# Kernel optimization log

Hardware: AMD Instinct MI355X
Metric: run time of the kernel (lower is better)

Reference implementation:

```python
import jax, jax.numpy as jnp
import numpy as np

B, T, N, H, DH = 32, 64, 100, 4, 32  # batch, seq, nodes, heads, dim/head


def setup_inputs() -> dict:
    key = jax.random.key(0)
    ks = jax.random.split(key, 20)
    # structured flat observation: [action_mask(132), adj(100*100), dt(1), obs(256), siem(128)]
    am = (jax.random.uniform(ks[0], (B, T, 132)) < 0.8).astype(jnp.float32)
    adj = (jax.random.uniform(ks[1], (B, T, N * N)) < 0.05).astype(jnp.float32)
    dt = jax.random.uniform(ks[2], (B, T, 1)) * 0.1 + 0.01
    obs = jax.random.normal(ks[3], (B, T, 256))
    siem = jax.random.normal(ks[4], (B, T, 128))
    inputs = jnp.concatenate([am, adj, dt, obs, siem], axis=-1)
    s = 0.05
    return dict(
        inputs=inputs,
        h0=jnp.zeros((B, 128), jnp.float32),
        fc_w=jax.random.normal(ks[5], (384, 256)) * s,
        fc_b=jnp.zeros((256,)),
        gat_w=jax.random.normal(ks[6], (256, H, DH)) * s,
        a_src=jax.random.normal(ks[7], (H, DH)) * s,
        a_dst=jax.random.normal(ks[8], (H, DH)) * s,
        ode_w1=jax.random.normal(ks[9], (128, 128)) * s,
        ode_b1=jnp.zeros((128,)),
        ode_w2=jax.random.normal(ks[10], (128, 128)) * s,
        ode_b2=jnp.zeros((128,)),
        gru_wi=jax.random.normal(ks[11], (128, 384)) * s,
        gru_wh=jax.random.normal(ks[12], (128, 384)) * s,
        gru_bi=jnp.zeros((384,)),
        gru_bh=jnp.zeros((384,)),
        act_w=jax.random.normal(ks[13], (128, 132)) * s,
        act_b=jnp.zeros((132,)),
        val_w=jax.random.normal(ks[14], (128, 1)) * s,
        val_b=jnp.zeros((1,)),
    )


def reference(inputs, h0, fc_w, fc_b, gat_w, a_src, a_dst, ode_w1, ode_b1,
              ode_w2, ode_b2, gru_wi, gru_wh, gru_bi, gru_bh, act_w, act_b,
              val_w, val_b):
    Bt, Tt = inputs.shape[0], inputs.shape[1]
    action_mask = inputs[..., :132]
    adj_raw = inputs[..., 132:10132].reshape(Bt * Tt, N, N)
    dtn = inputs[..., 10132:10133]                      # [B,T,1]
    x = jnp.concatenate([inputs[..., 10133:10389], inputs[..., 10389:10517]], -1)
    x = jax.nn.relu(x @ fc_w + fc_b).reshape(Bt * Tt, 256)
    # SubnetMaskGenerator.create_mask: binary adjacency + self loops
    adj = (adj_raw > 0) | jnp.eye(N, dtype=bool)[None]
    # place per-agent embedding at node 0, rest zero
    x_nodes = jnp.zeros((Bt * Tt, N, 256), x.dtype).at[:, 0, :].set(x)
    Wh = jnp.einsum('bnf,fhd->bhnd', x_nodes, gat_w)
    src = jnp.einsum('bhnd,hd->bhn', Wh, a_src)
    dst = jnp.einsum('bhnd,hd->bhn', Wh, a_dst)
    e = jax.nn.leaky_relu(src[:, :, :, None] + dst[:, :, None, :], 0.2)
    e = jnp.where(adj[:, None, :, :], e, -1e9)
    alpha = jax.nn.softmax(e, axis=-1)
    hgat = jax.nn.elu(jnp.einsum('bhij,bhjd->bhid', alpha, Wh))
    hgat = hgat.transpose(0, 2, 1, 3).reshape(Bt * Tt, N, H * DH)
    x_gat = hgat.mean(axis=1).reshape(Bt, Tt, 128)

    def f(h):  # ODE dynamics net
        return jnp.tanh(jnp.tanh(h @ ode_w1 + ode_b1) @ ode_w2 + ode_b2)

    def step(h, inp):
        xt, dt = inp                                    # [B,128], [B,1]
        k1 = f(h)
        k2 = f(h + 0.5 * dt * k1)
        k3 = f(h + 0.5 * dt * k2)
        k4 = f(h + dt * k3)
        h_ode = h + dt / 6.0 * (k1 + 2 * k2 + 2 * k3 + k4)
        gi = xt @ gru_wi + gru_bi
        gh = h_ode @ gru_wh + gru_bh
        ir, iz, inn = jnp.split(gi, 3, -1)
        hr, hz, hn = jnp.split(gh, 3, -1)
        r = jax.nn.sigmoid(ir + hr)
        z = jax.nn.sigmoid(iz + hz)
        n = jnp.tanh(inn + r * hn)
        h_new = (1.0 - z) * n + z * h_ode
        return h_new, h_new

    h_T, hs = jax.lax.scan(step, h0, (x_gat.transpose(1, 0, 2), dtn.transpose(1, 0, 2)))
    x_rnn = hs.transpose(1, 0, 2)                       # [B,T,128]
    logits = x_rnn @ act_w + act_b
    value = (x_rnn @ val_w + val_b).reshape(-1)
    masked_logits = jnp.where(action_mask == 0.0, jnp.float32(-1e10), logits)
    return masked_logits, h_T, value
```

## Files before the change

### kernel.cpp

```cpp
#include <hip/hip_runtime.h>

#define NIN 10517
typedef unsigned short ushort_t;
using f32x4  = __attribute__((ext_vector_type(4))) float;
using bf16x8 = __attribute__((ext_vector_type(8))) short;

__device__ __forceinline__ float lrelu02(float x){ return x > 0.f ? x : 0.2f*x; }
__device__ __forceinline__ float fast_tanh(float x){ float e=__expf(2.f*x); return 1.f - 2.f/(e+1.f); }
__device__ __forceinline__ float fast_sig(float x){ return 1.f/(1.f+__expf(-x)); }

__device__ __forceinline__ ushort_t f2bf(float x){
  unsigned u = __float_as_uint(x);
  unsigned r = u + 0x7FFF + ((u >> 16) & 1);
  return (ushort_t)(r >> 16);
}
__device__ __forceinline__ float bf2f(ushort_t v){ return __uint_as_float(((unsigned)v) << 16); }

#define LBAR() do { asm volatile("s_waitcnt lgkmcnt(0)" ::: "memory"); \
                    __builtin_amdgcn_s_barrier(); } while (0)

__global__ __launch_bounds__(256) void k_fc_gat(const float* __restrict__ inputs,
    const float* __restrict__ fc_w, const float* __restrict__ fc_b,
    const float* __restrict__ gat_w, const float* __restrict__ a_src, const float* __restrict__ a_dst,
    const float* __restrict__ ode_w1, const float* __restrict__ ode_w2, const float* __restrict__ gru_wh,
    const float* __restrict__ act_w, const float* __restrict__ gru_wi,
    float* __restrict__ wh0_ws, float* __restrict__ sd_ws,
    ushort_t* __restrict__ w1B, ushort_t* __restrict__ w2B, ushort_t* __restrict__ ghB,
    ushort_t* __restrict__ actB, ushort_t* __restrict__ wiBt,
    ushort_t* __restrict__ fc_wB, ushort_t* __restrict__ gat_wB)
{
  __shared__ __align__(16) ushort_t xinB[16][392];
  __shared__ __align__(16) ushort_t xfcB[16][264];
  __shared__ float wh[16][132];
  const int tid = threadIdx.x;
  const int bt0 = blockIdx.x * 16;

  for (int p = blockIdx.x * 256 + tid; p < 280576; p += 128*256) {
    if (p < 49152) {
      int m = p >> 7, k = p & 127;
      ghB[p] = f2bf(gru_wh[k*384 + m]);
    } else if (p < 65536) {
      int q = p - 49152, jj = q >> 7, k = q & 127;
      w1B[q] = f2bf(ode_w1[k*128 + jj]);
    } else if (p < 81920) {
      int q = p - 65536, jj = q >> 7, k = q & 127;
      w2B[q] = f2bf(ode_w2[k*128 + jj]);
    } else if (p < 100352) {
      int q = p - 81920, col = q >> 7, k = q & 127;
      actB[q] = (col < 132) ? f2bf(act_w[k*132 + col]) : (ushort_t)0;
    } else if (p < 149504) {
      int q = p - 100352, m = q >> 7, f = q & 127;
      wiBt[q] = f2bf(gru_wi[f*384 + m]);
    } else if (p < 247808) {
      int q = p - 149504, col = q / 384, k = q - col*384;
      fc_wB[q] = f2bf(fc_w[k*256 + col]);
    } else {
      int q = p - 247808, col = q >> 8, k = q & 255;
      gat_wB[q] = f2bf(gat_w[k*128 + col]);
    }
  }

  for (int idx = tid; idx < 16*384; idx += 256) {
    int r = idx / 384, f = idx - r*384;
    xinB[r][f] = f2bf(inputs[(size_t)(bt0+r)*NIN + 10133 + f]);
  }
  __syncthreads();

  const int w = tid >> 6, lane = tid & 63;
  const int li = lane & 15, g = lane >> 4;

  {
    bf16x8 afr[12];
    #pragma unroll
    for (int kt=0;kt<12;kt++)
      afr[kt] = *reinterpret_cast<const bf16x8*>(&xinB[li][kt*32 + g*8]);
    for (int ct = w*4; ct < w*4 + 4; ct++) {
      f32x4 acc = {0.f,0.f,0.f,0.f};
      #pragma unroll
      for (int kt=0;kt<12;kt++){
        bf16x8 bf = *reinterpret_cast<const bf16x8*>(fc_wB + (size_t)(ct*16+li)*384 + kt*32 + g*8);
        acc = __builtin_amdgcn_mfma_f32_16x16x32_bf16(afr[kt], bf, acc, 0,0,0);
      }
      const float bias = fc_b[ct*16 + li];
      #pragma unroll
      for (int r=0;r<4;r++)
        xfcB[g*4 + r][ct*16 + li] = f2bf(fmaxf(acc[r] + bias, 0.f));
    }
  }
  __syncthreads();

  {
    bf16x8 afr[8];
    #pragma unroll
    for (int kt=0;kt<8;kt++)
      afr[kt] = *reinterpret_cast<const bf16x8*>(&xfcB[li][kt*32 + g*8]);
    for (int ct = w*2; ct < w*2 + 2; ct++) {
      f32x4 acc = {0.f,0.f,0.f,0.f};
      #pragma unroll
      for (int kt=0;kt<8;kt++){
        bf16x8 bf = *reinterpret_cast<const bf16x8*>(gat_wB + (size_t)(ct*16+li)*256 + kt*32 + g*8);
        acc = __builtin_amdgcn_mfma_f32_16x16x32_bf16(afr[kt], bf, acc, 0,0,0);
      }
      #pragma unroll
      for (int r=0;r<4;r++){
        const int row = g*4 + r, col = ct*16 + li;
        wh[row][col] = acc[r];
        wh0_ws[(size_t)(bt0+row)*128 + col] = acc[r];
      }
    }
  }
  __syncthreads();

  if (tid < 128) {
    const int r = tid >> 3, h = (tid >> 1) & 3, wv = tid & 1;
    const float* av = wv ? a_dst : a_src;
    float acc = 0.f;
    #pragma unroll
    for (int d=0; d<32; d++) acc = fmaf(wh[r][h*32+d], av[h*32+d], acc);
    sd_ws[(size_t)(bt0+r)*8 + wv*4 + h] = acc;
  }
}

__global__ __launch_bounds__(256) void k_alpha_gi(const float* __restrict__ inputs,
    const float* __restrict__ wh0_ws, const float* __restrict__ sd_ws,
    ushort_t* __restrict__ xg_bf)
{
  __shared__ int cnt[100];
  __shared__ int a0f[100];
  __shared__ float alpha[4][100];
  __shared__ float wh0[128];
  __shared__ float sdl[8];
  __shared__ float psum[256];
  const int tid = threadIdx.x;
  const size_t bt = blockIdx.x;
  if (tid < 128) wh0[tid] = wh0_ws[bt*128 + tid];
  if (tid < 8) sdl[tid] = sd_ws[bt*8 + tid];
  const float* adj = inputs + bt*NIN + 132;
  const int wv = tid >> 6, lane = tid & 63;
  for (int i = wv; i < 100; i += 4) {
    float v0 = adj[i*100 + lane];
    int pred0 = (lane != 0) && ((v0 > 0.f) || (lane == i));
    unsigned long long b0 = __ballot(pred0);
    int pred1 = 0;
    if (lane < 36) {
      float v1 = adj[i*100 + 64 + lane];
      pred1 = (v1 > 0.f) || ((64 + lane) == i);
    }
    unsigned long long b1 = __ballot(pred1);
    if (lane == 0) {
      cnt[i] = __popcll(b0) + __popcll(b1);
      a0f[i] = (v0 > 0.f) ? 1 : 0;
    }
  }
  __syncthreads();
  for (int idx = tid; idx < 400; idx += 256) {
    int h = idx / 100, i = idx - h*100;
    float s = sdl[h], d = sdl[4+h];
    float a;
    if (i == 0) {
      float ea = __expf(lrelu02(s + d));
      float eb = __expf(lrelu02(s));
      a = ea / (ea + (float)cnt[0] * eb);
    } else if (a0f[i]) {
      float ed = __expf(lrelu02(d));
      a = ed / (ed + (float)cnt[i]);
    } else {
      a = 0.f;
    }
    alpha[h][i] = a;
  }
  __syncthreads();
  {
    const int pr = tid & 127, hf = tid >> 7;
    const float w = wh0[pr];
    const int hh = pr >> 5;
    float sum = 0.f;
    const int i0 = hf * 50;
    for (int i = i0; i < i0 + 50; i++) {
      float t = alpha[hh][i] * w;
      sum += (t > 0.f) ? t : (__expf(t) - 1.f);
    }
    psum[tid] = sum;
  }
  __syncthreads();
  if (tid < 128) xg_bf[bt*128 + tid] = f2bf((psum[tid] + psum[tid+128]) * 0.01f);
}

__global__ __launch_bounds__(256) void k_gi(const ushort_t* __restrict__ xg_bf,
    const ushort_t* __restrict__ wiBt, const float* __restrict__ gru_bi,
    float* __restrict__ gi_ws)
{
  const int tid = threadIdx.x;
  const int w = tid >> 6, lane = tid & 63;
  const int li = lane & 15, g = lane >> 4;
  const int bt0 = blockIdx.x * 16;
  bf16x8 haf[4];
  #pragma unroll
  for (int kt=0;kt<4;kt++)
    haf[kt] = *reinterpret_cast<const bf16x8*>(xg_bf + ((size_t)(bt0 + li))*128 + kt*32 + g*8);
  for (int ct = w*6; ct < w*6 + 6; ct++) {
    const int m = ct*16 + li;
    const f32x4 z0 = {0.f,0.f,0.f,0.f};
    const ushort_t* wb = wiBt + (size_t)m*128;
    bf16x8 b0 = *reinterpret_cast<const bf16x8*>(wb + 0*32 + g*8);
    bf16x8 b1f = *reinterpret_cast<const bf16x8*>(wb + 1*32 + g*8);
    bf16x8 b2f = *reinterpret_cast<const bf16x8*>(wb + 2*32 + g*8);
    bf16x8 b3f = *reinterpret_cast<const bf16x8*>(wb + 3*32 + g*8);
    f32x4 c0 = __builtin_amdgcn_mfma_f32_16x16x32_bf16(haf[0], b0,  z0, 0,0,0);
    f32x4 c1 = __builtin_amdgcn_mfma_f32_16x16x32_bf16(haf[1], b1f, z0, 0,0,0);
    f32x4 c2 = __builtin_amdgcn_mfma_f32_16x16x32_bf16(haf[2], b2f, z0, 0,0,0);
    f32x4 c3 = __builtin_amdgcn_mfma_f32_16x16x32_bf16(haf[3], b3f, z0, 0,0,0);
    const float bim = gru_bi[m];
    #pragma unroll
    for (int r=0;r<4;r++)
      gi_ws[(size_t)(bt0 + g*4 + r)*384 + m] = ((c0[r]+c1[r]) + (c2[r]+c3[r])) + bim;
  }
}

__global__ __launch_bounds__(512) void k_rnn(const float* __restrict__ inputs,
    const float* __restrict__ h0,
    const ushort_t* __restrict__ w1B, const float* __restrict__ ode_b1,
    const ushort_t* __restrict__ w2B, const float* __restrict__ ode_b2,
    const ushort_t* __restrict__ ghB, const float* __restrict__ gru_bh,
    const ushort_t* __restrict__ actB, const float* __restrict__ act_b,
    const float* __restrict__ val_w, const float* __restrict__ val_b,
    const float* __restrict__ gi_ws,
    float* __restrict__ out_logits, float* __restrict__ out_hT, float* __restrict__ out_val)
{
  __shared__ __align__(16) ushort_t bufA[128];
  __shared__ __align__(16) ushort_t bufB[128];
  __shared__ __align__(16) ushort_t bufC[128];
  __shared__ float dtbuf[64];
  __shared__ __align__(16) ushort_t hsbuf[64*136];
  const int tid = threadIdx.x;
  const int b = blockIdx.x;
  const int w = tid >> 6, lane = tid & 63;
  const int li = lane & 15, g = lane >> 4;
  const int col = w*16 + li;

  bf16x8 W1f[4], W2f[4], GAf[4], GBf[4], GCf[4];
  #pragma unroll
  for (int kt=0;kt<4;kt++){
    const int o = kt*32 + g*8;
    W1f[kt] = *reinterpret_cast<const bf16x8*>(w1B + col*128 + o);
    W2f[kt] = *reinterpret_cast<const bf16x8*>(w2B + col*128 + o);
    GAf[kt] = *reinterpret_cast<const bf16x8*>(ghB + (size_t)col*128       + o);
    GBf[kt] = *reinterpret_cast<const bf16x8*>(ghB + (size_t)(col+128)*128 + o);
    GCf[kt] = *reinterpret_cast<const bf16x8*>(ghB + (size_t)(col+256)*128 + o);
  }
  const float b1 = ode_b1[col], b2 = ode_b2[col];
  const float bh0 = gru_bh[col], bh1 = gru_bh[col+128], bh2 = gru_bh[col+256];
  float h = h0[b*128 + col];
  if (tid < 64) dtbuf[tid] = inputs[((size_t)b*64 + tid)*NIN + 10132];
  if (lane < 16) bufC[col] = f2bf(h);
  const float* gib = gi_ws + (size_t)b*64*384 + col;
  __syncthreads();

  bf16x8 af[4];
  auto ldaf = [&](const ushort_t* __restrict__ hb){
    #pragma unroll
    for (int kt=0;kt<4;kt++) af[kt] = *reinterpret_cast<const bf16x8*>(hb + kt*32 + g*8);
  };
  auto mvac = [&](const bf16x8 (&Wf)[4])->float{
    const f32x4 z0 = {0.f,0.f,0.f,0.f};
    f32x4 c0 = __builtin_amdgcn_mfma_f32_16x16x32_bf16(af[0], Wf[0], z0, 0,0,0);
    f32x4 c1 = __builtin_amdgcn_mfma_f32_16x16x32_bf16(af[1], Wf[1], z0, 0,0,0);
    f32x4 c2 = __builtin_amdgcn_mfma_f32_16x16x32_bf16(af[2], Wf[2], z0, 0,0,0);
    f32x4 c3 = __builtin_amdgcn_mfma_f32_16x16x32_bf16(af[3], Wf[3], z0, 0,0,0);
    return (c0[0]+c1[0]) + (c2[0]+c3[0]);
  };

  for (int t=0; t<64; t++) {
    const float dt = dtbuf[t];
    const float gir = gib[(size_t)t*384];
    const float giz = gib[(size_t)t*384 + 128];
    const float gin = gib[(size_t)t*384 + 256];

    float u, k1, k2, k3, k4;
    ldaf(bufC); u  = fast_tanh(mvac(W1f)+b1); if (lane<16) bufA[col]=f2bf(u);                    LBAR();
    ldaf(bufA); k1 = fast_tanh(mvac(W2f)+b2); if (lane<16) bufB[col]=f2bf(fmaf(0.5f*dt,k1,h));   LBAR();
    ldaf(bufB); u  = fast_tanh(mvac(W1f)+b1); if (lane<16) bufA[col]=f2bf(u);                    LBAR();
    ldaf(bufA); k2 = fast_tanh(mvac(W2f)+b2); if (lane<16) bufB[col]=f2bf(fmaf(0.5f*dt,k2,h));   LBAR();
    ldaf(bufB); u  = fast_tanh(mvac(W1f)+b1); if (lane<16) bufA[col]=f2bf(u);                    LBAR();
    ldaf(bufA); k3 = fast_tanh(mvac(W2f)+b2); if (lane<16) bufB[col]=f2bf(fmaf(dt,k3,h));        LBAR();
    ldaf(bufB); u  = fast_tanh(mvac(W1f)+b1); if (lane<16) bufA[col]=f2bf(u);                    LBAR();
    ldaf(bufA); k4 = fast_tanh(mvac(W2f)+b2);
    const float h_ode = fmaf(dt*(1.f/6.f), (k1 + 2.f*k2) + (2.f*k3 + k4), h);
    if (lane<16) bufB[col] = f2bf(h_ode);                                                        LBAR();

    ldaf(bufB);
    {
      const float r = fast_sig(gir + mvac(GAf) + bh0);
      const float z = fast_sig(giz + mvac(GBf) + bh1);
      const float n = fast_tanh(gin + r*(mvac(GCf) + bh2));
      h = (1.f - z)*n + z*h_ode;
    }
    if (lane < 16) {
      bufC[col] = f2bf(h);
      hsbuf[t*136 + col] = f2bf(h);
    }
    LBAR();
  }

  if (lane < 16) out_hT[b*128 + col] = h;

  {
    const int rt = w & 3, ch = w >> 2;
    const int r0 = rt*16;
    bf16x8 haf[4];
    #pragma unroll
    for (int kt=0;kt<4;kt++)
      haf[kt] = *reinterpret_cast<const bf16x8*>(hsbuf + (r0+li)*136 + kt*32 + g*8);
    const int ct0 = ch ? 5 : 0, ctN = ch ? 9 : 5;
    for (int ct=ct0; ct<ctN; ct++){
      const f32x4 z0 = {0.f,0.f,0.f,0.f};
      f32x4 c0, c1, c2, c3;
      {
        const ushort_t* ab = actB + (size_t)(ct*16+li)*128;
        bf16x8 b0 = *reinterpret_cast<const bf16x8*>(ab + 0*32 + g*8);
        bf16x8 b1f = *reinterpret_cast<const bf16x8*>(ab + 1*32 + g*8);
        bf16x8 b2f = *reinterpret_cast<const bf16x8*>(ab + 2*32 + g*8);
        bf16x8 b3f = *reinterpret_cast<const bf16x8*>(ab + 3*32 + g*8);
        c0 = __builtin_amdgcn_mfma_f32_16x16x32_bf16(haf[0], b0,  z0, 0,0,0);
        c1 = __builtin_amdgcn_mfma_f32_16x16x32_bf16(haf[1], b1f, z0, 0,0,0);
        c2 = __builtin_amdgcn_mfma_f32_16x16x32_bf16(haf[2], b2f, z0, 0,0,0);
        c3 = __builtin_amdgcn_mfma_f32_16x16x32_bf16(haf[3], b3f, z0, 0,0,0);
      }
      const int colL = ct*16 + li;
      if (colL < 132){
        const float ab = act_b[colL];
        #pragma unroll
        for (int reg=0; reg<4; reg++){
          const int r = r0 + g*4 + reg;
          const size_t bt = (size_t)b*64 + r;
          const float mval = inputs[bt*NIN + colL];
          const float v = ((c0[reg]+c1[reg]) + (c2[reg]+c3[reg])) + ab;
          out_logits[bt*132 + colL] = (mval == 0.f) ? -1e10f : v;
        }
      }
    }
  }
  if (tid < 64){
    float acc = val_b[0];
    for (int k=0;k<128;k++) acc = fmaf(bf2f(hsbuf[tid*136 + k]), val_w[k], acc);
    out_val[b*64 + tid] = acc;
  }
}

extern "C" void kernel_launch(void* const* d_in, const int* in_sizes, int n_in,
                              void* d_out, int out_size, void* d_ws, size_t ws_size,
                              hipStream_t stream) {
  (void)in_sizes; (void)n_in; (void)out_size; (void)ws_size;
  const float* inputs = (const float*)d_in[0];
  const float* h0     = (const float*)d_in[1];
  const float* fc_w   = (const float*)d_in[2];
  const float* fc_b   = (const float*)d_in[3];
  const float* gat_w  = (const float*)d_in[4];
  const float* a_src  = (const float*)d_in[5];
  const float* a_dst  = (const float*)d_in[6];
  const float* ode_w1 = (const float*)d_in[7];
  const float* ode_b1 = (const float*)d_in[8];
  const float* ode_w2 = (const float*)d_in[9];
  const float* ode_b2 = (const float*)d_in[10];
  const float* gru_wi = (const float*)d_in[11];
  const float* gru_wh = (const float*)d_in[12];
  const float* gru_bi = (const float*)d_in[13];
  const float* gru_bh = (const float*)d_in[14];
  const float* act_w  = (const float*)d_in[15];
  const float* act_b  = (const float*)d_in[16];
  const float* val_w  = (const float*)d_in[17];
  const float* val_b  = (const float*)d_in[18];

  float* ws   = (float*)d_ws;
  float* wh0  = ws;
  float* sd   = ws + 262144;
  ushort_t* xg_bf = (ushort_t*)(ws + 278528);
  float* gi   = ws + 409600;
  ushort_t* w1B   = (ushort_t*)(ws + 1196032);
  ushort_t* w2B   = (ushort_t*)(ws + 1204224);
  ushort_t* ghB   = (ushort_t*)(ws + 1212416);
  ushort_t* actB  = (ushort_t*)(ws + 1236992);
  ushort_t* wiBt  = (ushort_t*)(ws + 1246208);
  ushort_t* fc_wB = (ushort_t*)(ws + 1270784);
  ushort_t* gat_wB= (ushort_t*)(ws + 1319936);

  float* out        = (float*)d_out;
  float* out_logits = out;
  float* out_hT     = out + 270336;
  float* out_val    = out + 274432;

  k_fc_gat  <<<dim3(128),  dim3(256), 0, stream>>>(inputs, fc_w, fc_b, gat_w, a_src, a_dst,
                                                   ode_w1, ode_w2, gru_wh, act_w, gru_wi,
                                                   wh0, sd, w1B, w2B, ghB, actB, wiBt,
                                                   fc_wB, gat_wB);
  k_alpha_gi<<<dim3(2048), dim3(256), 0, stream>>>(inputs, wh0, sd, xg_bf);
  k_gi      <<<dim3(128),  dim3(256), 0, stream>>>(xg_bf, wiBt, gru_bi, gi);
  k_rnn     <<<dim3(32),   dim3(512), 0, stream>>>(inputs, h0, w1B, ode_b1, w2B, ode_b2,
                                                   ghB, gru_bh, actB, act_b, val_w, val_b,
                                                   gi, out_logits, out_hT, out_val);
}
```

Baseline: 205.1 us.

## Stream RNN weight fragments from cache per phase to cut registers and raise occupancy

```diff
diff --git a/kernel.cpp b/kernel.cpp
--- a/kernel.cpp
+++ b/kernel.cpp
@@ -217,7 +217,7 @@
   }
 }
 
-__global__ __launch_bounds__(512) void k_rnn(const float* __restrict__ inputs,
+__global__ __launch_bounds__(512, 2) void k_rnn(const float* __restrict__ inputs,
     const float* __restrict__ h0,
     const ushort_t* __restrict__ w1B, const float* __restrict__ ode_b1,
     const ushort_t* __restrict__ w2B, const float* __restrict__ ode_b2,
@@ -238,16 +238,12 @@
   const int li = lane & 15, g = lane >> 4;
   const int col = w*16 + li;
 
-  bf16x8 W1f[4], W2f[4], GAf[4], GBf[4], GCf[4];
-  #pragma unroll
-  for (int kt=0;kt<4;kt++){
-    const int o = kt*32 + g*8;
-    W1f[kt] = *reinterpret_cast<const bf16x8*>(w1B + col*128 + o);
-    W2f[kt] = *reinterpret_cast<const bf16x8*>(w2B + col*128 + o);
-    GAf[kt] = *reinterpret_cast<const bf16x8*>(ghB + (size_t)col*128       + o);
-    GBf[kt] = *reinterpret_cast<const bf16x8*>(ghB + (size_t)(col+128)*128 + o);
-    GCf[kt] = *reinterpret_cast<const bf16x8*>(ghB + (size_t)(col+256)*128 + o);
-  }
+  const ushort_t* p_w1 = w1B + col*128;
+  const ushort_t* p_w2 = w2B + col*128;
+  const ushort_t* p_ga = ghB + (size_t)col*128;
+  const ushort_t* p_gb = ghB + (size_t)(col+128)*128;
+  const ushort_t* p_gc = ghB + (size_t)(col+256)*128;
+
   const float b1 = ode_b1[col], b2 = ode_b2[col];
   const float bh0 = gru_bh[col], bh1 = gru_bh[col+128], bh2 = gru_bh[col+256];
   float h = h0[b*128 + col];
@@ -260,6 +256,10 @@
   auto ldaf = [&](const ushort_t* __restrict__ hb){
     #pragma unroll
     for (int kt=0;kt<4;kt++) af[kt] = *reinterpret_cast<const bf16x8*>(hb + kt*32 + g*8);
+  };
+  auto ldw = [&](bf16x8 (&d)[4], const ushort_t* __restrict__ src){
+    #pragma unroll
+    for (int kt=0;kt<4;kt++) d[kt] = *reinterpret_cast<const bf16x8*>(src + kt*32 + g*8);
   };
   auto mvac = [&](const bf16x8 (&Wf)[4])->float{
     const f32x4 z0 = {0.f,0.f,0.f,0.f};
@@ -270,6 +270,9 @@
     return (c0[0]+c1[0]) + (c2[0]+c3[0]);
   };
 
+  bf16x8 Wa[4], Wb[4], GAf[4], GBf[4], GCf[4];
+  ldw(Wa, p_w1);
+
   for (int t=0; t<64; t++) {
     const float dt = dtbuf[t];
     const float gir = gib[(size_t)t*384];
@@ -277,18 +280,18 @@
     const float gin = gib[(size_t)t*384 + 256];
 
     float u, k1, k2, k3, k4;
-    ldaf(bufC); u  = fast_tanh(mvac(W1f)+b1); if (lane<16) bufA[col]=f2bf(u);                    LBAR();
-    ldaf(bufA); k1 = fast_tanh(mvac(W2f)+b2); if (lane<16) bufB[col]=f2bf(fmaf(0.5f*dt,k1,h));   LBAR();
-    ldaf(bufB); u  = fast_tanh(mvac(W1f)+b1); if (lane<16) bufA[col]=f2bf(u);                    LBAR();
-    ldaf(bufA); k2 = fast_tanh(mvac(W2f)+b2); if (lane<16) bufB[col]=f2bf(fmaf(0.5f*dt,k2,h));   LBAR();
-    ldaf(bufB); u  = fast_tanh(mvac(W1f)+b1); if (lane<16) bufA[col]=f2bf(u);                    LBAR();
-    ldaf(bufA); k3 = fast_tanh(mvac(W2f)+b2); if (lane<16) bufB[col]=f2bf(fmaf(dt,k3,h));        LBAR();
-    ldaf(bufB); u  = fast_tanh(mvac(W1f)+b1); if (lane<16) bufA[col]=f2bf(u);                    LBAR();
-    ldaf(bufA); k4 = fast_tanh(mvac(W2f)+b2);
+    ldaf(bufC); ldw(Wb, p_w2); u  = fast_tanh(mvac(Wa)+b1); if (lane<16) bufA[col]=f2bf(u);                  LBAR();
+    ldaf(bufA); ldw(Wa, p_w1); k1 = fast_tanh(mvac(Wb)+b2); if (lane<16) bufB[col]=f2bf(fmaf(0.5f*dt,k1,h)); LBAR();
+    ldaf(bufB); ldw(Wb, p_w2); u  = fast_tanh(mvac(Wa)+b1); if (lane<16) bufA[col]=f2bf(u);                  LBAR();
+    ldaf(bufA); ldw(Wa, p_w1); k2 = fast_tanh(mvac(Wb)+b2); if (lane<16) bufB[col]=f2bf(fmaf(0.5f*dt,k2,h)); LBAR();
+    ldaf(bufB); ldw(Wb, p_w2); u  = fast_tanh(mvac(Wa)+b1); if (lane<16) bufA[col]=f2bf(u);                  LBAR();
+    ldaf(bufA); ldw(Wa, p_w1); k3 = fast_tanh(mvac(Wb)+b2); if (lane<16) bufB[col]=f2bf(fmaf(dt,k3,h));      LBAR();
+    ldaf(bufB); ldw(Wb, p_w2); u  = fast_tanh(mvac(Wa)+b1); if (lane<16) bufA[col]=f2bf(u);                  LBAR();
+    ldaf(bufA); ldw(GAf, p_ga); ldw(GBf, p_gb); ldw(GCf, p_gc);
+    k4 = fast_tanh(mvac(Wb)+b2);
     const float h_ode = fmaf(dt*(1.f/6.f), (k1 + 2.f*k2) + (2.f*k3 + k4), h);
-    if (lane<16) bufB[col] = f2bf(h_ode);                                                        LBAR();
-
-    ldaf(bufB);
+    if (lane<16) bufB[col] = f2bf(h_ode);                                                                    LBAR();
+    ldaf(bufB); ldw(Wa, p_w1);
     {
       const float r = fast_sig(gir + mvac(GAf) + bh0);
       const float z = fast_sig(giz + mvac(GBf) + bh1);
```

Result: slower. 346.4 us (+68.9%).
